# Kernel optimization log

Measured on AMD Instinct MI355X. Metric: run time of the kernel, lower is better.

## Reference

```python
import jax, jax.numpy as jnp
import numpy as np

N_NODES = 50000
N_EDGES = 800000
IN_F, HID, HEADS, OUT_F = 64, 64, 4, 64
NEG_SLOPE = 0.2


def _gat_conv(x, ei, W, a_src, a_dst, b, H, C):
    """PyG-style GATConv (eval mode, add_self_loops=True, concat=True).
    x: [N, F_in], ei: [2, E], W: [F_in, H*C], a_src/a_dst: [H, C], b: [H*C].
    """
    N = x.shape[0]
    h = (x @ W).reshape(N, H, C)                      # [N,H,C]
    asrc = jnp.einsum('nhc,hc->nh', h, a_src)         # [N,H]
    adst = jnp.einsum('nhc,hc->nh', h, a_dst)         # [N,H]
    src, dst = ei[0], ei[1]
    logits = jax.nn.leaky_relu(asrc[src] + adst[dst], NEG_SLOPE)  # [E,H]
    m = jax.ops.segment_max(logits, dst, num_segments=N)
    m = jnp.where(jnp.isfinite(m), m, 0.0)
    ex = jnp.exp(logits - m[dst])
    denom = jax.ops.segment_sum(ex, dst, num_segments=N)
    alpha = ex / (denom[dst] + 1e-16)                 # [E,H]
    msg = h[src] * alpha[:, :, None]                  # [E,H,C]
    out = jax.ops.segment_sum(msg, dst, num_segments=N)  # [N,H,C]
    return out.reshape(N, H * C) + b


def _add_self_loops(ei, n):
    loops = jnp.arange(n, dtype=ei.dtype)
    return jnp.concatenate([ei, jnp.stack([loops, loops])], axis=1)


def setup_inputs() -> dict:
    key = jax.random.key(0)
    ks = jax.random.split(key, 16)
    x = jax.random.normal(ks[0], (N_NODES, IN_F), dtype=jnp.float32)
    edge_index = jax.random.randint(ks[1], (2, N_EDGES), 0, N_NODES, dtype=jnp.int32)
    s = 0.1
    d = {'x': x, 'edge_index': edge_index}
    # layer 0: IN_F -> HID, HEADS heads
    d['W0'] = jax.random.normal(ks[2], (IN_F, HEADS * HID), jnp.float32) * s
    d['a_src0'] = jax.random.normal(ks[3], (HEADS, HID), jnp.float32) * s
    d['a_dst0'] = jax.random.normal(ks[4], (HEADS, HID), jnp.float32) * s
    d['b0'] = jnp.zeros((HEADS * HID,), jnp.float32)
    # layer 1: HEADS*HID -> HID, HEADS heads
    d['W1'] = jax.random.normal(ks[5], (HEADS * HID, HEADS * HID), jnp.float32) * s
    d['a_src1'] = jax.random.normal(ks[6], (HEADS, HID), jnp.float32) * s
    d['a_dst1'] = jax.random.normal(ks[7], (HEADS, HID), jnp.float32) * s
    d['b1'] = jnp.zeros((HEADS * HID,), jnp.float32)
    # layer 2: HEADS*HID -> OUT_F, 1 head
    d['W2'] = jax.random.normal(ks[8], (HEADS * HID, OUT_F), jnp.float32) * s
    d['a_src2'] = jax.random.normal(ks[9], (1, OUT_F), jnp.float32) * s
    d['a_dst2'] = jax.random.normal(ks[10], (1, OUT_F), jnp.float32) * s
    d['b2'] = jnp.zeros((OUT_F,), jnp.float32)
    return d


def reference(x, edge_index, W0, a_src0, a_dst0, b0, W1, a_src1, a_dst1, b1, W2, a_src2, a_dst2, b2):
    ei = _add_self_loops(edge_index, x.shape[0])
    h = _gat_conv(x, ei, W0, a_src0, a_dst0, b0, HEADS, HID)
    h = jax.nn.elu(h)  # dropout identity in eval
    h = _gat_conv(h, ei, W1, a_src1, a_dst1, b1, HEADS, HID)
    h = jax.nn.elu(h)
    out = _gat_conv(h, ei, W2, a_src2, a_dst2, b2, 1, OUT_F)
    return out
```

## Files before the change

kernel.cpp:

```cpp
#include <hip/hip_runtime.h>
#include <hip/hip_fp16.h>
#include <math.h>

#define NODES 50000
#define EDGES 800000
#define NB_SCAN ((NODES + 1023) / 1024)

typedef __attribute__((ext_vector_type(8))) _Float16 f16x8;
typedef __attribute__((ext_vector_type(4))) _Float16 f16x4;
typedef __attribute__((ext_vector_type(4))) float f32x4;

__device__ __forceinline__ float lrelu02(float x){ return x > 0.f ? x : 0.2f * x; }

__device__ __forceinline__ f32x4 shflx4(f32x4 v, int m){
  f32x4 r;
  r[0] = __shfl_xor(v[0], m); r[1] = __shfl_xor(v[1], m);
  r[2] = __shfl_xor(v[2], m); r[3] = __shfl_xor(v[3], m);
  return r;
}


__global__ __launch_bounds__(256) void gat_zero(int* __restrict__ p, int n){
  int i = blockIdx.x * 256 + threadIdx.x;
  if (i < n) p[i] = 0;
}

__global__ __launch_bounds__(256) void gat_hist(const int* __restrict__ ei, int* __restrict__ cnt){
  int e = blockIdx.x * 256 + threadIdx.x;
  if (e < EDGES) atomicAdd(&cnt[ei[EDGES + e]], 1);
}

__global__ __launch_bounds__(256) void gat_blocksum(const int* __restrict__ cnt, int* __restrict__ bsums){
  __shared__ int sd[256];
  int t = threadIdx.x, b = blockIdx.x;
  int base = b * 1024 + t * 4, s = 0;
  #pragma unroll
  for (int j = 0; j < 4; j++){ int i = base + j; if (i < NODES) s += cnt[i]; }
  sd[t] = s; __syncthreads();
  for (int o = 128; o > 0; o >>= 1){ if (t < o) sd[t] += sd[t + o]; __syncthreads(); }
  if (t == 0) bsums[b] = sd[0];
}

__global__ void gat_scan_bsums(int* bsums, int nb){
  if (threadIdx.x == 0 && blockIdx.x == 0){
    int run = 0;
    for (int i = 0; i < nb; i++){ int v = bsums[i]; bsums[i] = run; run += v; }
  }
}

__global__ __launch_bounds__(256) void gat_rowptr(int* __restrict__ cnt, const int* __restrict__ bsums,
                                                  int* __restrict__ row_ptr){
  __shared__ int sd[256];
  int t = threadIdx.x, b = blockIdx.x;
  int base = b * 1024 + t * 4;
  int c[4]; int s = 0;
  #pragma unroll
  for (int j = 0; j < 4; j++){
    int i = base + j;
    c[j] = (i < NODES) ? cnt[i] : 0;
    s += c[j];
    if (i < NODES) cnt[i] = 0;
  }
  sd[t] = s; __syncthreads();
  for (int o = 1; o < 256; o <<= 1){
    int v = (t >= o) ? sd[t - o] : 0;
    __syncthreads();
    if (t >= o) sd[t] += v;
    __syncthreads();
  }
  int off = bsums[b] + sd[t] - s;
  #pragma unroll
  for (int j = 0; j < 4; j++){
    int i = base + j;
    if (i < NODES){ row_ptr[i] = off; off += c[j]; }
  }
  if (b == 0 && t == 0) row_ptr[NODES] = EDGES;
}

__global__ __launch_bounds__(256) void gat_scatter(const int* __restrict__ ei, const int* __restrict__ row_ptr,
                                                    int* __restrict__ fill, int* __restrict__ col,
                                                    int* __restrict__ dstarr){
  int e = blockIdx.x * 256 + threadIdx.x;
  if (e < EDGES){
    int s = ei[e], d = ei[EDGES + e];
    int pos = row_ptr[d] + atomicAdd(&fill[d], 1);
    col[pos] = s;
    dstarr[pos] = d;
  }
}


__global__ __launch_bounds__(256) void gat_prep(const float* __restrict__ x, _Float16* __restrict__ xh,
                                                const float* __restrict__ W0, const float* __restrict__ W1,
                                                const float* __restrict__ W2,
                                                _Float16* __restrict__ Wt0, _Float16* __restrict__ Wt1,
                                                _Float16* __restrict__ Wt2,
                                                const float* __restrict__ as0, const float* __restrict__ ad0,
                                                float* __restrict__ ws, float* __restrict__ wd){
  int b = blockIdx.x;
  int t = threadIdx.x;
  if (b < 3125){
    int i = b * 256 + t;
    float4 v = *(const float4*)(x + (size_t)i * 4);
    f16x4 h = { (_Float16)v.x, (_Float16)v.y, (_Float16)v.z, (_Float16)v.w };
    *(f16x4*)(xh + (size_t)i * 4) = h;
  } else if (b < 3701){
    int k = b - 3125;
    if (k < 64){
      Wt0[(size_t)t * 64 + k] = (_Float16)W0[(size_t)k * 256 + t];
    } else if (k < 320){
      int kk = k - 64;
      Wt1[(size_t)t * 256 + kk] = (_Float16)W1[(size_t)kk * 256 + t];
    } else {
      int kk = k - 320;
      if (t < 64) Wt2[(size_t)t * 256 + kk] = (_Float16)W2[(size_t)kk * 64 + t];
    }
  } else {
    int h = t >> 6, c = t & 63;
    float s = 0.f, d = 0.f;
    for (int cc = 0; cc < 64; cc++){
      float w = W0[(size_t)c * 256 + h * 64 + cc];
      s += w * as0[h * 64 + cc];
      d += w * ad0[h * 64 + cc];
    }
    ws[h * 64 + c] = s;
    wd[h * 64 + c] = d;
  }
}


template<int K, int N, int ATTN>
__global__ __launch_bounds__(256) void gat_gemm_mfma(const _Float16* __restrict__ A, const _Float16* __restrict__ Wt,
                                                      _Float16* __restrict__ C,
                                                      const float* __restrict__ a_srcv, const float* __restrict__ a_dstv,
                                                      float* __restrict__ asrc, float* __restrict__ adst, int M){
  constexpr int NT = N / 64;
  constexpr int LDT = 40;
  __shared__ _Float16 As[64][LDT];
  __shared__ _Float16 Bs[N][LDT];

  int tid = threadIdx.x;
  int w = tid >> 6, l = tid & 63;
  int lg = l >> 4, lr = l & 15;
  int bm = blockIdx.x * 64;

  f32x4 acc[4][NT];
  #pragma unroll
  for (int m = 0; m < 4; m++)
    #pragma unroll
    for (int n = 0; n < NT; n++)
      acc[m][n] = (f32x4){0.f, 0.f, 0.f, 0.f};

  int ar = tid >> 2;
  int akc = (tid & 3) * 8;
  bool avalid = (bm + ar) < M;
  const _Float16* aptr = A + (size_t)(bm + ar) * K + akc;

  for (int k0 = 0; k0 < K; k0 += 32){
    float4 av = avalid ? *(const float4*)(aptr + k0) : make_float4(0.f, 0.f, 0.f, 0.f);
    __syncthreads();
    *(float4*)&As[ar][akc] = av;
    #pragma unroll
    for (int c = 0; c < N / 64; c++){
      int idx = c * 256 + tid;
      int n = idx >> 2, kc = (idx & 3) * 8;
      *(float4*)&Bs[n][kc] = *(const float4*)(Wt + (size_t)n * K + k0 + kc);
    }
    __syncthreads();

    f16x8 af[4], bf[NT];
    #pragma unroll
    for (int m = 0; m < 4; m++) af[m] = *(const f16x8*)&As[16 * m + lr][8 * lg];
    #pragma unroll
    for (int n = 0; n < NT; n++) bf[n] = *(const f16x8*)&Bs[w * (N / 4) + 16 * n + lr][8 * lg];
    #pragma unroll
    for (int m = 0; m < 4; m++)
      #pragma unroll
      for (int n = 0; n < NT; n++)
        acc[m][n] = __builtin_amdgcn_mfma_f32_16x16x32_f16(af[m], bf[n], acc[m][n], 0, 0, 0);
  }

  #pragma unroll
  for (int m = 0; m < 4; m++){
    #pragma unroll
    for (int j = 0; j < 4; j++){
      int row = bm + 16 * m + 4 * lg + j;
      if (row < M){
        #pragma unroll
        for (int n = 0; n < NT; n++)
          C[(size_t)row * N + w * (N / 4) + 16 * n + lr] = (_Float16)acc[m][n][j];
      }
    }
  }

  if constexpr (ATTN == 4){
    float avs[4], avd[4];
    #pragma unroll
    for (int n = 0; n < 4; n++){
      avs[n] = a_srcv[w * 64 + 16 * n + lr];
      avd[n] = a_dstv[w * 64 + 16 * n + lr];
    }
    #pragma unroll
    for (int m = 0; m < 4; m++){
      #pragma unroll
      for (int j = 0; j < 4; j++){
        float s1 = acc[m][0][j] * avs[0] + acc[m][1][j] * avs[1] + acc[m][2][j] * avs[2] + acc[m][3][j] * avs[3];
        float s2 = acc[m][0][j] * avd[0] + acc[m][1][j] * avd[1] + acc[m][2][j] * avd[2] + acc[m][3][j] * avd[3];
        #pragma unroll
        for (int o = 8; o > 0; o >>= 1){ s1 += __shfl_xor(s1, o); s2 += __shfl_xor(s2, o); }
        int row = bm + 16 * m + 4 * lg + j;
        if (lr == 0 && row < M){
          asrc[row * 4 + w] = s1;
          adst[row * 4 + w] = s2;
        }
      }
    }
  }
  if constexpr (ATTN == 1){
    __shared__ float sred[2][4][64];
    float av = a_srcv[w * 16 + lr], dv = a_dstv[w * 16 + lr];
    #pragma unroll
    for (int m = 0; m < 4; m++){
      #pragma unroll
      for (int j = 0; j < 4; j++){
        float s1 = acc[m][0][j] * av;
        float s2 = acc[m][0][j] * dv;
        #pragma unroll
        for (int o = 8; o > 0; o >>= 1){ s1 += __shfl_xor(s1, o); s2 += __shfl_xor(s2, o); }
        if (lr == 0){
          sred[0][w][16 * m + 4 * lg + j] = s1;
          sred[1][w][16 * m + 4 * lg + j] = s2;
        }
      }
    }
    __syncthreads();
    if (tid < 64){
      int row = bm + tid;
      if (row < M){
        asrc[row] = sred[0][0][tid] + sred[0][1][tid] + sred[0][2][tid] + sred[0][3][tid];
        adst[row] = sred[1][0][tid] + sred[1][1][tid] + sred[1][2][tid] + sred[1][3][tid];
      }
    }
  }
}


__global__ __launch_bounds__(256) void gat_gemm_bd(const _Float16* __restrict__ A, const _Float16* __restrict__ Bt,
                                                    const float* __restrict__ bias, _Float16* __restrict__ C, int M){
  int tid = threadIdx.x;
  int w = tid >> 6, l = tid & 63;
  int lg = l >> 4, lr = l & 15;
  int bm = blockIdx.x * 64;

  f32x4 acc[4][4];
  #pragma unroll
  for (int m = 0; m < 4; m++)
    #pragma unroll
    for (int n = 0; n < 4; n++)
      acc[m][n] = (f32x4){0.f, 0.f, 0.f, 0.f};

  f16x8 zf = {};
  #pragma unroll
  for (int ks = 0; ks < 2; ks++){
    int koff = ks * 32;
    f16x8 af[4], bf[4];
    #pragma unroll
    for (int m = 0; m < 4; m++){
      int row = bm + 16 * m + lr;
      af[m] = (row < M) ? *(const f16x8*)(A + (size_t)row * 256 + w * 64 + koff + 8 * lg) : zf;
    }
    #pragma unroll
    for (int n = 0; n < 4; n++)
      bf[n] = *(const f16x8*)(Bt + (size_t)(w * 64 + 16 * n + lr) * 64 + koff + 8 * lg);
    #pragma unroll
    for (int m = 0; m < 4; m++)
      #pragma unroll
      for (int n = 0; n < 4; n++)
        acc[m][n] = __builtin_amdgcn_mfma_f32_16x16x32_f16(af[m], bf[n], acc[m][n], 0, 0, 0);
  }

  #pragma unroll
  for (int m = 0; m < 4; m++){
    #pragma unroll
    for (int j = 0; j < 4; j++){
      int row = bm + 16 * m + 4 * lg + j;
      if (row < M){
        #pragma unroll
        for (int n = 0; n < 4; n++){
          int cc = w * 64 + 16 * n + lr;
          float o = acc[m][n][j] + bias[cc];
          o = o > 0.f ? o : expm1f(o);
          C[(size_t)row * 256 + cc] = (_Float16)o;
        }
      }
    }
  }
}


__global__ __launch_bounds__(256) void gat_attn0(const _Float16* __restrict__ xh, const float* __restrict__ ws,
                                                  const float* __restrict__ wd,
                                                  float* __restrict__ asrc, float* __restrict__ adst, int N){
  int lane = threadIdx.x & 63;
  int wid = threadIdx.x >> 6;
  int n = blockIdx.x * 4 + wid;
  if (n >= N) return;
  float v = (float)xh[(size_t)n * 64 + lane];
  #pragma unroll
  for (int h = 0; h < 4; h++){
    float s1 = v * ws[h * 64 + lane];
    float s2 = v * wd[h * 64 + lane];
    #pragma unroll
    for (int o = 32; o > 0; o >>= 1){ s1 += __shfl_xor(s1, o); s2 += __shfl_xor(s2, o); }
    if (lane == 0){ asrc[n * 4 + h] = s1; adst[n * 4 + h] = s2; }
  }
}


__global__ __launch_bounds__(256) void gat_edge_exp0(const int* __restrict__ col, const int* __restrict__ dstarr,
                                                      const float* __restrict__ asrc, const float* __restrict__ adst,
                                                      float* __restrict__ exf){
  int i = blockIdx.x * 256 + threadIdx.x;
  if (i >= EDGES) return;
  int s = col[i], d = dstarr[i];
  float4 a = *(const float4*)&asrc[s * 4];
  float4 b = *(const float4*)&adst[d * 4];
  float4 r;
  r.x = __expf(lrelu02(a.x + b.x));
  r.y = __expf(lrelu02(a.y + b.y));
  r.z = __expf(lrelu02(a.z + b.z));
  r.w = __expf(lrelu02(a.w + b.w));
  *(float4*)&exf[(size_t)i * 4] = r;
}


__global__ __launch_bounds__(256) void gat_aggregate_in64(const _Float16* __restrict__ xh, const float* __restrict__ exf,
                                                           const float* __restrict__ asrc, const float* __restrict__ adst,
                                                           const int* __restrict__ row_ptr, const int* __restrict__ col,
                                                           _Float16* __restrict__ agg){
  int lane = threadIdx.x & 63;
  int wid = threadIdx.x >> 6;
  int d = blockIdx.x * 4 + wid;
  if (d >= NODES) return;
  int slot = lane >> 4;
  int cpos = (lane & 15) * 4;

  f32x4 acc0 = {0,0,0,0}, acc1 = {0,0,0,0}, acc2 = {0,0,0,0}, acc3 = {0,0,0,0};
  f32x4 den = {0,0,0,0};

  int e0 = row_ptr[d], e1 = row_ptr[d + 1];
  const _Float16* xb = xh + cpos;
  int e = e0;
  for (; e + 8 <= e1; e += 8){
    int eA = e + slot, eB = e + 4 + slot;
    int sA = col[eA], sB = col[eB];
    float4 fA = *(const float4*)(exf + (size_t)eA * 4);
    float4 fB = *(const float4*)(exf + (size_t)eB * 4);
    f16x4 hA = *(const f16x4*)(xb + (size_t)sA * 64);
    f16x4 hB = *(const f16x4*)(xb + (size_t)sB * 64);
    f32x4 vA = { (float)hA[0], (float)hA[1], (float)hA[2], (float)hA[3] };
    f32x4 vB = { (float)hB[0], (float)hB[1], (float)hB[2], (float)hB[3] };
    den += (f32x4){ fA.x + fB.x, fA.y + fB.y, fA.z + fB.z, fA.w + fB.w };
    acc0 += fA.x * vA + fB.x * vB;
    acc1 += fA.y * vA + fB.y * vB;
    acc2 += fA.z * vA + fB.z * vB;
    acc3 += fA.w * vA + fB.w * vB;
  }
  if (e + 4 <= e1){
    int eA = e + slot;
    int sA = col[eA];
    float4 fA = *(const float4*)(exf + (size_t)eA * 4);
    f16x4 hA = *(const f16x4*)(xb + (size_t)sA * 64);
    f32x4 vA = { (float)hA[0], (float)hA[1], (float)hA[2], (float)hA[3] };
    den += (f32x4){ fA.x, fA.y, fA.z, fA.w };
    acc0 += fA.x * vA; acc1 += fA.y * vA; acc2 += fA.z * vA; acc3 += fA.w * vA;
    e += 4;
  }
  {
    int eA = e + slot;
    if (eA < e1){
      int sA = col[eA];
      float4 fA = *(const float4*)(exf + (size_t)eA * 4);
      f16x4 hA = *(const f16x4*)(xb + (size_t)sA * 64);
      f32x4 vA = { (float)hA[0], (float)hA[1], (float)hA[2], (float)hA[3] };
      den += (f32x4){ fA.x, fA.y, fA.z, fA.w };
      acc0 += fA.x * vA; acc1 += fA.y * vA; acc2 += fA.z * vA; acc3 += fA.w * vA;
    }
  }

  #pragma unroll
  for (int off = 16; off <= 32; off <<= 1){
    acc0 += shflx4(acc0, off);
    acc1 += shflx4(acc1, off);
    acc2 += shflx4(acc2, off);
    acc3 += shflx4(acc3, off);
    den  += shflx4(den,  off);
  }

  float4 a4 = *(const float4*)&asrc[d * 4];
  float4 b4 = *(const float4*)&adst[d * 4];
  float es0 = __expf(lrelu02(a4.x + b4.x));
  float es1 = __expf(lrelu02(a4.y + b4.y));
  float es2 = __expf(lrelu02(a4.z + b4.z));
  float es3 = __expf(lrelu02(a4.w + b4.w));
  f16x4 hs = *(const f16x4*)(xh + (size_t)d * 64 + cpos);
  f32x4 vs = { (float)hs[0], (float)hs[1], (float)hs[2], (float)hs[3] };
  acc0 += es0 * vs; acc1 += es1 * vs; acc2 += es2 * vs; acc3 += es3 * vs;
  den += (f32x4){ es0, es1, es2, es3 };

  if (slot == 0){
    float i0 = 1.f / (den[0] + 1e-16f), i1 = 1.f / (den[1] + 1e-16f);
    float i2 = 1.f / (den[2] + 1e-16f), i3 = 1.f / (den[3] + 1e-16f);
    _Float16* ob = agg + (size_t)d * 256 + cpos;
    f16x4 o0 = { (_Float16)(acc0[0]*i0), (_Float16)(acc0[1]*i0), (_Float16)(acc0[2]*i0), (_Float16)(acc0[3]*i0) };
    f16x4 o1 = { (_Float16)(acc1[0]*i1), (_Float16)(acc1[1]*i1), (_Float16)(acc1[2]*i1), (_Float16)(acc1[3]*i1) };
    f16x4 o2 = { (_Float16)(acc2[0]*i2), (_Float16)(acc2[1]*i2), (_Float16)(acc2[2]*i2), (_Float16)(acc2[3]*i2) };
    f16x4 o3 = { (_Float16)(acc3[0]*i3), (_Float16)(acc3[1]*i3), (_Float16)(acc3[2]*i3), (_Float16)(acc3[3]*i3) };
    *(f16x4*)(ob)       = o0;
    *(f16x4*)(ob + 64)  = o1;
    *(f16x4*)(ob + 128) = o2;
    *(f16x4*)(ob + 192) = o3;
  }
}


__global__ __launch_bounds__(256) void gat_aggregate4(const _Float16* __restrict__ hH, const float* __restrict__ asrc,
                                                       const float* __restrict__ adst,
                                                       const int* __restrict__ row_ptr, const int* __restrict__ col,
                                                       const float* __restrict__ bias, _Float16* __restrict__ out){
  int lane = threadIdx.x & 63;
  int wid = threadIdx.x >> 6;
  int d = blockIdx.x * 4 + wid;
  if (d >= NODES) return;
  int q = lane >> 4;
  int co = lane * 4;

  float adq = adst[d * 4 + q];

  float ex = __expf(lrelu02(asrc[d * 4 + q] + adq));
  f16x4 hv = *(const f16x4*)(hH + (size_t)d * 256 + co);
  float4 acc = make_float4(ex * (float)hv[0], ex * (float)hv[1], ex * (float)hv[2], ex * (float)hv[3]);
  float den = ex;

  int e0 = row_ptr[d], e1 = row_ptr[d + 1];
  const _Float16* hbase = hH + co;
  int e = e0;
  for (; e + 4 <= e1; e += 4){
    int s0 = col[e], s1 = col[e + 1], s2 = col[e + 2], s3 = col[e + 3];
    float a0 = asrc[s0 * 4 + q], a1 = asrc[s1 * 4 + q], a2 = asrc[s2 * 4 + q], a3 = asrc[s3 * 4 + q];
    f16x4 h0 = *(const f16x4*)(hbase + (size_t)s0 * 256);
    f16x4 h1 = *(const f16x4*)(hbase + (size_t)s1 * 256);
    f16x4 h2 = *(const f16x4*)(hbase + (size_t)s2 * 256);
    f16x4 h3 = *(const f16x4*)(hbase + (size_t)s3 * 256);
    float x0 = __expf(lrelu02(a0 + adq));
    float x1 = __expf(lrelu02(a1 + adq));
    float x2 = __expf(lrelu02(a2 + adq));
    float x3 = __expf(lrelu02(a3 + adq));
    den += x0 + x1 + x2 + x3;
    acc.x += x0 * (float)h0[0] + x1 * (float)h1[0] + x2 * (float)h2[0] + x3 * (float)h3[0];
    acc.y += x0 * (float)h0[1] + x1 * (float)h1[1] + x2 * (float)h2[1] + x3 * (float)h3[1];
    acc.z += x0 * (float)h0[2] + x1 * (float)h1[2] + x2 * (float)h2[2] + x3 * (float)h3[2];
    acc.w += x0 * (float)h0[3] + x1 * (float)h1[3] + x2 * (float)h2[3] + x3 * (float)h3[3];
  }
  for (; e < e1; e++){
    int s0 = col[e];
    float a0 = asrc[s0 * 4 + q];
    f16x4 h0 = *(const f16x4*)(hbase + (size_t)s0 * 256);
    float x0 = __expf(lrelu02(a0 + adq));
    den += x0;
    acc.x += x0 * (float)h0[0]; acc.y += x0 * (float)h0[1];
    acc.z += x0 * (float)h0[2]; acc.w += x0 * (float)h0[3];
  }

  float inv = 1.f / (den + 1e-16f);
  float4 b4 = *(const float4*)&bias[co];
  float4 o = make_float4(acc.x * inv + b4.x, acc.y * inv + b4.y, acc.z * inv + b4.z, acc.w * inv + b4.w);
  o.x = o.x > 0.f ? o.x : expm1f(o.x);
  o.y = o.y > 0.f ? o.y : expm1f(o.y);
  o.z = o.z > 0.f ? o.z : expm1f(o.z);
  o.w = o.w > 0.f ? o.w : expm1f(o.w);
  f16x4 oh = { (_Float16)o.x, (_Float16)o.y, (_Float16)o.z, (_Float16)o.w };
  *(f16x4*)(out + (size_t)d * 256 + co) = oh;
}


__global__ __launch_bounds__(256) void gat_aggregate1n(const _Float16* __restrict__ hH,
                                                        const float* __restrict__ asrc, const float* __restrict__ adst,
                                                        const int* __restrict__ row_ptr, const int* __restrict__ col,
                                                        const float* __restrict__ bias, float* __restrict__ out){
  int lane = threadIdx.x & 63;
  int wid = threadIdx.x >> 6;
  int d = blockIdx.x * 4 + wid;
  if (d >= NODES) return;
  int slot = lane >> 4;
  int cpos = (lane & 15) * 4;

  float adq = adst[d];
  f32x4 acc = {0,0,0,0};
  float den = 0.f;

  int e0 = row_ptr[d], e1 = row_ptr[d + 1];
  const _Float16* hb = hH + cpos;
  int e = e0;
  for (; e + 8 <= e1; e += 8){
    int eA = e + slot, eB = e + 4 + slot;
    int sA = col[eA], sB = col[eB];
    float fA = __expf(lrelu02(asrc[sA] + adq));
    float fB = __expf(lrelu02(asrc[sB] + adq));
    f16x4 hA = *(const f16x4*)(hb + (size_t)sA * 64);
    f16x4 hB = *(const f16x4*)(hb + (size_t)sB * 64);
    f32x4 vA = { (float)hA[0], (float)hA[1], (float)hA[2], (float)hA[3] };
    f32x4 vB = { (float)hB[0], (float)hB[1], (float)hB[2], (float)hB[3] };
    den += fA + fB;
    acc += fA * vA + fB * vB;
  }
  if (e + 4 <= e1){
    int eA = e + slot;
    int sA = col[eA];
    float fA = __expf(lrelu02(asrc[sA] + adq));
    f16x4 hA = *(const f16x4*)(hb + (size_t)sA * 64);
    f32x4 vA = { (float)hA[0], (float)hA[1], (float)hA[2], (float)hA[3] };
    den += fA; acc += fA * vA;
    e += 4;
  }
  {
    int eA = e + slot;
    if (eA < e1){
      int sA = col[eA];
      float fA = __expf(lrelu02(asrc[sA] + adq));
      f16x4 hA = *(const f16x4*)(hb + (size_t)sA * 64);
      f32x4 vA = { (float)hA[0], (float)hA[1], (float)hA[2], (float)hA[3] };
      den += fA; acc += fA * vA;
    }
  }

  #pragma unroll
  for (int off = 16; off <= 32; off <<= 1){
    acc += shflx4(acc, off);
    den += __shfl_xor(den, off);
  }

  float es = __expf(lrelu02(asrc[d] + adq));
  f16x4 hs = *(const f16x4*)(hH + (size_t)d * 64 + cpos);
  f32x4 vs = { (float)hs[0], (float)hs[1], (float)hs[2], (float)hs[3] };
  acc += es * vs;
  den += es;

  if (slot == 0){
    float inv = 1.f / (den + 1e-16f);
    float4 b4 = *(const float4*)&bias[cpos];
    float4 o = make_float4(acc[0] * inv + b4.x, acc[1] * inv + b4.y, acc[2] * inv + b4.z, acc[3] * inv + b4.w);
    *(float4*)(out + (size_t)d * 64 + cpos) = o;
  }
}


extern "C" void kernel_launch(void* const* d_in, const int* in_sizes, int n_in,
                              void* d_out, int out_size, void* d_ws, size_t ws_size,
                              hipStream_t stream) {
  const float* x   = (const float*)d_in[0];
  const int*   ei  = (const int*)  d_in[1];
  const float* W0  = (const float*)d_in[2];
  const float* as0 = (const float*)d_in[3];
  const float* ad0 = (const float*)d_in[4];
  const float* b0  = (const float*)d_in[5];
  const float* W1  = (const float*)d_in[6];
  const float* as1 = (const float*)d_in[7];
  const float* ad1 = (const float*)d_in[8];
  const float* b1  = (const float*)d_in[9];
  const float* W2  = (const float*)d_in[10];
  const float* as2 = (const float*)d_in[11];
  const float* ad2 = (const float*)d_in[12];
  const float* b2  = (const float*)d_in[13];
  float* out = (float*)d_out;

  auto al = [](size_t v){ return (v + 255) & ~(size_t)255; };
  char* p = (char*)d_ws;
  int*      row_ptr = (int*)p;      p += al((NODES + 1) * sizeof(int));
  int*      cnt     = (int*)p;      p += al(NODES * sizeof(int));
  int*      bsums   = (int*)p;      p += al(64 * sizeof(int));
  int*      col     = (int*)p;      p += al(EDGES * sizeof(int));
  int*      dstarr  = (int*)p;      p += al(EDGES * sizeof(int));
  float*    exf     = (float*)p;    p += al((size_t)EDGES * 4 * sizeof(float));
  float*    asrc    = (float*)p;    p += al(NODES * 4 * sizeof(float));
  float*    adst    = (float*)p;    p += al(NODES * 4 * sizeof(float));
  _Float16* xh      = (_Float16*)p; p += al((size_t)NODES * 64 * sizeof(_Float16));
  _Float16* hH      = (_Float16*)p; p += al((size_t)NODES * 256 * sizeof(_Float16));
  _Float16* actb    = (_Float16*)p; p += al((size_t)NODES * 256 * sizeof(_Float16));
  _Float16* Wt0     = (_Float16*)p; p += al(256 * 64 * sizeof(_Float16));
  _Float16* Wt1     = (_Float16*)p; p += al(256 * 256 * sizeof(_Float16));
  _Float16* Wt2     = (_Float16*)p; p += al(64 * 256 * sizeof(_Float16));
  float*    ws0     = (float*)p;    p += al(256 * sizeof(float));
  float*    wd0     = (float*)p;    p += al(256 * sizeof(float));

  gat_prep<<<3702, 256, 0, stream>>>(x, xh, W0, W1, W2, Wt0, Wt1, Wt2, as0, ad0, ws0, wd0);

  gat_zero<<<(NODES + 255) / 256, 256, 0, stream>>>(cnt, NODES);
  gat_hist<<<(EDGES + 255) / 256, 256, 0, stream>>>(ei, cnt);
  gat_blocksum<<<NB_SCAN, 256, 0, stream>>>(cnt, bsums);
  gat_scan_bsums<<<1, 64, 0, stream>>>(bsums, NB_SCAN);
  gat_rowptr<<<NB_SCAN, 256, 0, stream>>>(cnt, bsums, row_ptr);
  gat_scatter<<<(EDGES + 255) / 256, 256, 0, stream>>>(ei, row_ptr, cnt, col, dstarr);

  const int nodeBlocks = (NODES + 3) / 4;
  const int gemmBlocks = (NODES + 63) / 64;
  const int edgeBlocks = (EDGES + 255) / 256;

  gat_attn0<<<nodeBlocks, 256, 0, stream>>>(xh, ws0, wd0, asrc, adst, NODES);
  gat_edge_exp0<<<edgeBlocks, 256, 0, stream>>>(col, dstarr, asrc, adst, exf);
  gat_aggregate_in64<<<nodeBlocks, 256, 0, stream>>>(xh, exf, asrc, adst, row_ptr, col, hH);
  gat_gemm_bd<<<gemmBlocks, 256, 0, stream>>>(hH, Wt0, b0, actb, NODES);

  gat_gemm_mfma<256, 256, 4><<<gemmBlocks, 256, 0, stream>>>(actb, Wt1, hH, as1, ad1, asrc, adst, NODES);
  gat_aggregate4<<<nodeBlocks, 256, 0, stream>>>(hH, asrc, adst, row_ptr, col, b1, actb);

  gat_gemm_mfma<256, 64, 1><<<gemmBlocks, 256, 0, stream>>>(actb, Wt2, hH, as2, ad2, asrc, adst, NODES);
  gat_aggregate1n<<<nodeBlocks, 256, 0, stream>>>(hH, asrc, adst, row_ptr, col, b2, out);
}
```

Baseline: 347.1 us.

## Load MFMA GEMM operands directly from global and fold small prep kernels

The MFMA GEMM drops its shared-memory staging and the two barriers per k-step. Each lane now loads its A and B fragments straight from global memory and relies on cache for reuse across waves. The zeroing of the count array moves into extra blocks of the prep kernel, and the single-thread block-sum scan is replaced by each rowptr block summing the preceding block totals itself. Together these remove two launches and the LDS synchronisation, at the cost of redundant global/L2 fragment loads across the four waves of a block.

```diff
diff --git a/kernel.cpp b/kernel.cpp
--- a/kernel.cpp
+++ b/kernel.cpp
@@ -20,11 +20,6 @@
 }
 
 
-__global__ __launch_bounds__(256) void gat_zero(int* __restrict__ p, int n){
-  int i = blockIdx.x * 256 + threadIdx.x;
-  if (i < n) p[i] = 0;
-}
-
 __global__ __launch_bounds__(256) void gat_hist(const int* __restrict__ ei, int* __restrict__ cnt){
   int e = blockIdx.x * 256 + threadIdx.x;
   if (e < EDGES) atomicAdd(&cnt[ei[EDGES + e]], 1);
@@ -39,13 +34,6 @@
   sd[t] = s; __syncthreads();
   for (int o = 128; o > 0; o >>= 1){ if (t < o) sd[t] += sd[t + o]; __syncthreads(); }
   if (t == 0) bsums[b] = sd[0];
-}
-
-__global__ void gat_scan_bsums(int* bsums, int nb){
-  if (threadIdx.x == 0 && blockIdx.x == 0){
-    int run = 0;
-    for (int i = 0; i < nb; i++){ int v = bsums[i]; bsums[i] = run; run += v; }
-  }
 }
 
 __global__ __launch_bounds__(256) void gat_rowptr(int* __restrict__ cnt, const int* __restrict__ bsums,
@@ -68,7 +56,9 @@
     if (t >= o) sd[t] += v;
     __syncthreads();
   }
-  int off = bsums[b] + sd[t] - s;
+  int pre = 0;
+  for (int i = 0; i < b; i++) pre += bsums[i];
+  int off = pre + sd[t] - s;
   #pragma unroll
   for (int j = 0; j < 4; j++){
     int i = base + j;
@@ -96,7 +86,8 @@
                                                 _Float16* __restrict__ Wt0, _Float16* __restrict__ Wt1,
                                                 _Float16* __restrict__ Wt2,
                                                 const float* __restrict__ as0, const float* __restrict__ ad0,
-                                                float* __restrict__ ws, float* __restrict__ wd){
+                                                float* __restrict__ ws, float* __restrict__ wd,
+                                                int* __restrict__ cnt){
   int b = blockIdx.x;
   int t = threadIdx.x;
   if (b < 3125){
@@ -115,7 +106,7 @@
       int kk = k - 320;
       if (t < 64) Wt2[(size_t)t * 256 + kk] = (_Float16)W2[(size_t)kk * 64 + t];
     }
-  } else {
+  } else if (b == 3701){
     int h = t >> 6, c = t & 63;
     float s = 0.f, d = 0.f;
     for (int cc = 0; cc < 64; cc++){
@@ -125,20 +116,19 @@
     }
     ws[h * 64 + c] = s;
     wd[h * 64 + c] = d;
+  } else {
+    int i = (b - 3702) * 256 + t;
+    if (i < NODES) cnt[i] = 0;
   }
 }
 
 
 template<int K, int N, int ATTN>
-__global__ __launch_bounds__(256) void gat_gemm_mfma(const _Float16* __restrict__ A, const _Float16* __restrict__ Wt,
-                                                      _Float16* __restrict__ C,
-                                                      const float* __restrict__ a_srcv, const float* __restrict__ a_dstv,
-                                                      float* __restrict__ asrc, float* __restrict__ adst, int M){
+__global__ __launch_bounds__(256) void gat_gemm_nolds(const _Float16* __restrict__ A, const _Float16* __restrict__ Wt,
+                                                       _Float16* __restrict__ C,
+                                                       const float* __restrict__ a_srcv, const float* __restrict__ a_dstv,
+                                                       float* __restrict__ asrc, float* __restrict__ adst, int M){
   constexpr int NT = N / 64;
-  constexpr int LDT = 40;
-  __shared__ _Float16 As[64][LDT];
-  __shared__ _Float16 Bs[N][LDT];
-
   int tid = threadIdx.x;
   int w = tid >> 6, l = tid & 63;
   int lg = l >> 4, lr = l & 15;
@@ -151,28 +141,26 @@
     for (int n = 0; n < NT; n++)
       acc[m][n] = (f32x4){0.f, 0.f, 0.f, 0.f};
 
-  int ar = tid >> 2;
-  int akc = (tid & 3) * 8;
-  bool avalid = (bm + ar) < M;
-  const _Float16* aptr = A + (size_t)(bm + ar) * K + akc;
-
+  const _Float16* ap[4];
+  bool avalid[4];
+  #pragma unroll
+  for (int m = 0; m < 4; m++){
+    int row = bm + 16 * m + lr;
+    avalid[m] = row < M;
+    ap[m] = A + (size_t)(avalid[m] ? row : 0) * K + 8 * lg;
+  }
+  const _Float16* bp[NT];
+  #pragma unroll
+  for (int n = 0; n < NT; n++)
+    bp[n] = Wt + (size_t)(w * (N / 4) + 16 * n + lr) * K + 8 * lg;
+
+  f16x8 zf = {};
   for (int k0 = 0; k0 < K; k0 += 32){
-    float4 av = avalid ? *(const float4*)(aptr + k0) : make_float4(0.f, 0.f, 0.f, 0.f);
-    __syncthreads();
-    *(float4*)&As[ar][akc] = av;
-    #pragma unroll
-    for (int c = 0; c < N / 64; c++){
-      int idx = c * 256 + tid;
-      int n = idx >> 2, kc = (idx & 3) * 8;
-      *(float4*)&Bs[n][kc] = *(const float4*)(Wt + (size_t)n * K + k0 + kc);
-    }
-    __syncthreads();
-
     f16x8 af[4], bf[NT];
     #pragma unroll
-    for (int m = 0; m < 4; m++) af[m] = *(const f16x8*)&As[16 * m + lr][8 * lg];
-    #pragma unroll
-    for (int n = 0; n < NT; n++) bf[n] = *(const f16x8*)&Bs[w * (N / 4) + 16 * n + lr][8 * lg];
+    for (int m = 0; m < 4; m++) af[m] = avalid[m] ? *(const f16x8*)(ap[m] + k0) : zf;
+    #pragma unroll
+    for (int n = 0; n < NT; n++) bf[n] = *(const f16x8*)(bp[n] + k0);
     #pragma unroll
     for (int m = 0; m < 4; m++)
       #pragma unroll
@@ -593,12 +581,10 @@
   float*    ws0     = (float*)p;    p += al(256 * sizeof(float));
   float*    wd0     = (float*)p;    p += al(256 * sizeof(float));
 
-  gat_prep<<<3702, 256, 0, stream>>>(x, xh, W0, W1, W2, Wt0, Wt1, Wt2, as0, ad0, ws0, wd0);
-
-  gat_zero<<<(NODES + 255) / 256, 256, 0, stream>>>(cnt, NODES);
+  gat_prep<<<3898, 256, 0, stream>>>(x, xh, W0, W1, W2, Wt0, Wt1, Wt2, as0, ad0, ws0, wd0, cnt);
+
   gat_hist<<<(EDGES + 255) / 256, 256, 0, stream>>>(ei, cnt);
   gat_blocksum<<<NB_SCAN, 256, 0, stream>>>(cnt, bsums);
-  gat_scan_bsums<<<1, 64, 0, stream>>>(bsums, NB_SCAN);
   gat_rowptr<<<NB_SCAN, 256, 0, stream>>>(cnt, bsums, row_ptr);
   gat_scatter<<<(EDGES + 255) / 256, 256, 0, stream>>>(ei, row_ptr, cnt, col, dstarr);
 
@@ -611,9 +597,9 @@
   gat_aggregate_in64<<<nodeBlocks, 256, 0, stream>>>(xh, exf, asrc, adst, row_ptr, col, hH);
   gat_gemm_bd<<<gemmBlocks, 256, 0, stream>>>(hH, Wt0, b0, actb, NODES);
 
-  gat_gemm_mfma<256, 256, 4><<<gemmBlocks, 256, 0, stream>>>(actb, Wt1, hH, as1, ad1, asrc, adst, NODES);
+  gat_gemm_nolds<256, 256, 4><<<gemmBlocks, 256, 0, stream>>>(actb, Wt1, hH, as1, ad1, asrc, adst, NODES);
   gat_aggregate4<<<nodeBlocks, 256, 0, stream>>>(hH, asrc, adst, row_ptr, col, b1, actb);
 
-  gat_gemm_mfma<256, 64, 1><<<gemmBlocks, 256, 0, stream>>>(actb, Wt2, hH, as2, ad2, asrc, adst, NODES);
+  gat_gemm_nolds<256, 64, 1><<<gemmBlocks, 256, 0, stream>>>(actb, Wt2, hH, as2, ad2, asrc, adst, NODES);
   gat_aggregate1n<<<nodeBlocks, 256, 0, stream>>>(hH, asrc, adst, row_ptr, col, b2, out);
 }
```

New measurement: 365.1 us. 5.2% more time.
